# Kernel optimization log

Hardware: AMD Instinct MI355X
Metric: run time of the kernel (lower is better)

## Reference

```python
import jax, jax.numpy as jnp
import numpy as np

N, C, H, W = 8, 256, 128, 128
HW = H * W
NB = 20            # boxes per image
TEMP = 0.5
RATIO = 1.0
IMG_H, IMG_W = 800.0, 800.0  # img_metas[i]['img_shape']


def setup_inputs() -> dict:
    key = jax.random.key(0)
    k1, k2, k3 = jax.random.split(key, 3)
    preds_S = jax.random.normal(k1, (HW, N, C), dtype=jnp.float32)
    preds_T = jax.random.normal(k2, (HW, N, C), dtype=jnp.float32)
    # boxes: random corner pairs in image coords, sorted so x1<=x2, y1<=y2
    u = jax.random.uniform(k3, (N, NB, 4), dtype=jnp.float32)
    x1 = jnp.minimum(u[..., 0], u[..., 2]) * IMG_W
    x2 = jnp.maximum(u[..., 0], u[..., 2]) * IMG_W
    y1 = jnp.minimum(u[..., 1], u[..., 3]) * IMG_H
    y2 = jnp.maximum(u[..., 1], u[..., 3]) * IMG_H
    gt_bboxes = jnp.stack([x1, y1, x2, y2], axis=-1)  # (N, NB, 4)
    return {"preds_S": preds_S, "preds_T": preds_T, "gt_bboxes": gt_bboxes}


def get_attention(preds, temp):
    # preds: (N, C, H, W)
    value = jnp.abs(preds)
    fea_map = value.mean(axis=1)                                   # (N, H, W)
    S_att = (H * W) * jax.nn.softmax((fea_map / temp).reshape(N, -1), axis=1)
    S_att = S_att.reshape(N, H, W)
    channel_map = value.mean(axis=(2, 3))                          # (N, C)
    C_att = C * jax.nn.softmax(channel_map / temp, axis=1)
    return S_att, C_att


def build_masks(gt_bboxes):
    # boxes scaled to feature grid (same math as torch loop, vectorized)
    wmin = jnp.floor(gt_bboxes[..., 0] / IMG_W * W).astype(jnp.int32)  # (N, NB)
    wmax = jnp.ceil(gt_bboxes[..., 2] / IMG_W * W).astype(jnp.int32)
    hmin = jnp.floor(gt_bboxes[..., 1] / IMG_H * H).astype(jnp.int32)
    hmax = jnp.ceil(gt_bboxes[..., 3] / IMG_H * H).astype(jnp.int32)
    area = 1.0 / (hmax + 1 - hmin).astype(jnp.float32) / (wmax + 1 - wmin).astype(jnp.float32)
    hh = jnp.arange(H)[None, None, :, None]
    ww = jnp.arange(W)[None, None, None, :]
    inside = ((hh >= hmin[:, :, None, None]) & (hh <= hmax[:, :, None, None]) &
              (ww >= wmin[:, :, None, None]) & (ww <= wmax[:, :, None, None]))  # (N, NB, H, W)
    # per-box max-scatter == max over boxes of (area where inside else 0)
    Mask_fg = jnp.max(jnp.where(inside, area[:, :, None, None], 0.0), axis=1)  # (N, H, W)
    Mask_bg = (Mask_fg <= 0).astype(jnp.float32)
    s = Mask_bg.sum(axis=(1, 2), keepdims=True)
    Mask_bg = jnp.where(s > 0, Mask_bg / s, Mask_bg)
    return Mask_fg, Mask_bg


def reference(preds_S, preds_T, gt_bboxes):
    # attention from DETACHED teacher features (preds_T.detach() in torch)
    pT_det = jax.lax.stop_gradient(preds_T)
    pT_new = pT_det.reshape(H, W, N, C).transpose(2, 3, 0, 1)  # (N, C, H, W)
    S_t, C_t = get_attention(pT_new, TEMP)

    Mask_fg, Mask_bg = build_masks(gt_bboxes)

    # flatten to the (HW, bs, .) layout of get_fea_loss
    flat = lambda m: m.transpose(1, 2, 0).reshape(HW, N, 1)
    S_t_f = flat(S_t)
    Mfg_f = flat(Mask_fg)
    Mbg_f = flat(Mask_bg)
    C_t_f = C_t[None]  # (1, bs, c) broadcast

    w = jnp.sqrt(S_t_f) * jnp.sqrt(C_t_f)
    fea_t = preds_T * w
    fea_s = preds_S * w
    diff = jnp.abs(fea_s - fea_t)
    fg_loss = jnp.sum(diff * jnp.sqrt(Mfg_f)) / HW
    bg_loss = jnp.sum(diff * jnp.sqrt(Mbg_f)) / HW
    return (fg_loss + bg_loss) * RATIO
```

## Files before the change

### kernel.cpp

```cpp
#include <hip/hip_runtime.h>

#define N_   8
#define C_   256
#define H_   128
#define W_   128
#define HW_  16384
#define NB_  20
constexpr float TEMP  = 0.5f;
constexpr float IMG_W = 800.0f;
constexpr float IMG_H = 800.0f;

__device__ __forceinline__ float waveReduceSum(float v) {
    v += __shfl_xor(v, 32, 64);
    v += __shfl_xor(v, 16, 64);
    v += __shfl_xor(v, 8, 64);
    v += __shfl_xor(v, 4, 64);
    v += __shfl_xor(v, 2, 64);
    v += __shfl_xor(v, 1, 64);
    return v;
}

__global__ __launch_bounds__(256) void k_stats(const float* __restrict__ pT,
                                               float* __restrict__ chan_sum,
                                               float* __restrict__ fea_sum) {
    const int n    = blockIdx.x & 7;
    const int p    = blockIdx.x >> 3;
    const int wave = threadIdx.x >> 6;
    const int lane = threadIdx.x & 63;
    float4 cacc = make_float4(0.f, 0.f, 0.f, 0.f);
    const int hw0 = p * 256 + wave * 64;
    for (int i = 0; i < 64; ++i) {
        const int hw = hw0 + i;
        const float4 v = *(const float4*)(pT + ((size_t)(hw * N_ + n)) * C_ + lane * 4);
        const float ax = fabsf(v.x), ay = fabsf(v.y), az = fabsf(v.z), aw = fabsf(v.w);
        cacc.x += ax; cacc.y += ay; cacc.z += az; cacc.w += aw;
        const float s = waveReduceSum(ax + ay + az + aw);
        if (lane == 0) fea_sum[n * HW_ + hw] = s;
    }
    __shared__ float lds[4][C_];
    lds[wave][lane * 4 + 0] = cacc.x;
    lds[wave][lane * 4 + 1] = cacc.y;
    lds[wave][lane * 4 + 2] = cacc.z;
    lds[wave][lane * 4 + 3] = cacc.w;
    __syncthreads();
    const int c = threadIdx.x;
    const float v = lds[0][c] + lds[1][c] + lds[2][c] + lds[3][c];
    atomicAdd(&chan_sum[n * C_ + c], v);
}

__global__ __launch_bounds__(256) void k_soft(const float* __restrict__ fea_sum,
                                              const float* __restrict__ chan_sum,
                                              float* __restrict__ stats,
                                              float* __restrict__ B) {
    const int n = blockIdx.x;
    const int tid = threadIdx.x;
    __shared__ float red[256];
    float m = -1e30f;
    for (int i = tid; i < HW_; i += 256) m = fmaxf(m, fea_sum[n * HW_ + i]);
    red[tid] = m; __syncthreads();
    for (int s = 128; s > 0; s >>= 1) { if (tid < s) red[tid] = fmaxf(red[tid], red[tid + s]); __syncthreads(); }
    const float smax = red[0] * (1.0f / (C_ * TEMP));
    __syncthreads();
    float acc = 0.f;
    for (int i = tid; i < HW_; i += 256)
        acc += expf(fea_sum[n * HW_ + i] * (1.0f / (C_ * TEMP)) - smax);
    red[tid] = acc; __syncthreads();
    for (int s = 128; s > 0; s >>= 1) { if (tid < s) red[tid] += red[tid + s]; __syncthreads(); }
    const float sden = red[0];
    __syncthreads();
    const float lc = chan_sum[n * C_ + tid] * (1.0f / (HW_ * TEMP));
    red[tid] = lc; __syncthreads();
    for (int s = 128; s > 0; s >>= 1) { if (tid < s) red[tid] = fmaxf(red[tid], red[tid + s]); __syncthreads(); }
    const float cmax = red[0]; __syncthreads();
    const float e = expf(lc - cmax);
    red[tid] = e; __syncthreads();
    for (int s = 128; s > 0; s >>= 1) { if (tid < s) red[tid] += red[tid + s]; __syncthreads(); }
    const float cden = red[0];
    B[n * C_ + tid] = sqrtf((float)C_ * e / cden);
    if (tid == 0) { stats[n] = smax; stats[N_ + n] = sden; }
}

__global__ __launch_bounds__(256) void k_mask(const float* __restrict__ gt,
                                              float* __restrict__ Mfg,
                                              float* __restrict__ bgcnt) {
    const int n = blockIdx.y;
    const int hw = blockIdx.x * 256 + threadIdx.x;
    const int h = hw >> 7, w = hw & 127;
    float fg = 0.f;
    for (int b = 0; b < NB_; ++b) {
        const float* bx = gt + ((size_t)n * NB_ + b) * 4;
        const float x1 = bx[0], y1 = bx[1], x2 = bx[2], y2 = bx[3];
        const int wmin = (int)floorf(x1 / IMG_W * (float)W_);
        const int wmax = (int)ceilf (x2 / IMG_W * (float)W_);
        const int hmin = (int)floorf(y1 / IMG_H * (float)H_);
        const int hmax = (int)ceilf (y2 / IMG_H * (float)H_);
        if (h >= hmin && h <= hmax && w >= wmin && w <= wmax) {
            const float area = 1.0f / (float)(hmax + 1 - hmin) / (float)(wmax + 1 - wmin);
            fg = fmaxf(fg, area);
        }
    }
    Mfg[n * HW_ + hw] = fg;
    __shared__ float red[256];
    red[threadIdx.x] = (fg <= 0.f) ? 1.f : 0.f;
    __syncthreads();
    for (int s = 128; s > 0; s >>= 1) { if (threadIdx.x < s) red[threadIdx.x] += red[threadIdx.x + s]; __syncthreads(); }
    if (threadIdx.x == 0) atomicAdd(&bgcnt[n], red[0]);
}

__global__ __launch_bounds__(256) void k_A(const float* __restrict__ fea_sum,
                                           const float* __restrict__ Mfg,
                                           const float* __restrict__ bgcnt,
                                           const float* __restrict__ stats,
                                           float* __restrict__ A) {
    const int n = blockIdx.y;
    const int hw = blockIdx.x * 256 + threadIdx.x;
    const float smax = stats[n], sden = stats[N_ + n];
    const float logit = fea_sum[n * HW_ + hw] * (1.0f / (C_ * TEMP));
    const float S_att = (float)HW_ * expf(logit - smax) / sden;
    const float fg = Mfg[n * HW_ + hw];
    const float s = bgcnt[n];
    const float bg = (fg <= 0.f) ? ((s > 0.f) ? 1.0f / s : 1.0f) : 0.f;
    A[n * HW_ + hw] = sqrtf(S_att) * (sqrtf(fg) + sqrtf(bg)) * (1.0f / (float)HW_);
}

__global__ __launch_bounds__(256) void k_main(const float* __restrict__ pS,
                                              const float* __restrict__ pT,
                                              const float* __restrict__ A,
                                              const float* __restrict__ B,
                                              float* __restrict__ partials) {
    const int wave = threadIdx.x >> 6, lane = threadIdx.x & 63;
    const int wg = blockIdx.x * 4 + wave;
    const int n = wg & 7;
    const int widx = wg >> 3;
    const float4 B4 = *(const float4*)(B + n * C_ + lane * 4);
    float acc = 0.f;
    const int hw0 = widx * 32;
    for (int i = 0; i < 32; ++i) {
        const int hw = hw0 + i;
        const size_t off = ((size_t)(hw * N_ + n)) * C_ + lane * 4;
        const float4 sv = *(const float4*)(pS + off);
        const float4 tv = *(const float4*)(pT + off);
        const float part = fabsf(sv.x - tv.x) * B4.x + fabsf(sv.y - tv.y) * B4.y +
                           fabsf(sv.z - tv.z) * B4.z + fabsf(sv.w - tv.w) * B4.w;
        acc += A[n * HW_ + hw] * part;
    }
    acc = waveReduceSum(acc);
    __shared__ float red[4];
    if (lane == 0) red[wave] = acc;
    __syncthreads();
    if (threadIdx.x == 0) partials[blockIdx.x] = red[0] + red[1] + red[2] + red[3];
}

__global__ __launch_bounds__(256) void k_final(const float* __restrict__ partials,
                                               float* __restrict__ out) {
    float a = 0.f;
    for (int i = threadIdx.x; i < 1024; i += 256) a += partials[i];
    __shared__ float red[256];
    red[threadIdx.x] = a; __syncthreads();
    for (int s = 128; s > 0; s >>= 1) { if (threadIdx.x < s) red[threadIdx.x] += red[threadIdx.x + s]; __syncthreads(); }
    if (threadIdx.x == 0) out[0] = red[0];
}

extern "C" void kernel_launch(void* const* d_in, const int* in_sizes, int n_in,
                              void* d_out, int out_size, void* d_ws, size_t ws_size,
                              hipStream_t stream) {
    const float* pS = (const float*)d_in[0];
    const float* pT = (const float*)d_in[1];
    const float* gt = (const float*)d_in[2];
    float* ws = (float*)d_ws;

    float* chan_sum = ws;
    float* bgcnt    = ws + 2048;
    float* stats    = ws + 2056;
    float* fea_sum  = ws + 4096;
    float* Mfg      = fea_sum + N_ * HW_;
    float* A        = Mfg + N_ * HW_;
    float* B        = A + N_ * HW_;
    float* partials = B + N_ * C_;

    hipMemsetAsync(ws, 0, 2056 * sizeof(float), stream);

    k_stats<<<512, 256, 0, stream>>>(pT, chan_sum, fea_sum);
    k_soft<<<N_, 256, 0, stream>>>(fea_sum, chan_sum, stats, B);
    k_mask<<<dim3(HW_ / 256, N_), 256, 0, stream>>>(gt, Mfg, bgcnt);
    k_A<<<dim3(HW_ / 256, N_), 256, 0, stream>>>(fea_sum, Mfg, bgcnt, stats, A);
    k_main<<<1024, 256, 0, stream>>>(pS, pT, A, B, partials);
    k_final<<<1, 256, 0, stream>>>(partials, (float*)d_out);
}
```

Before: 338.9 us.

## Fuse mask and attention prep into stats/main kernels, parallelize softmax reductions

Mask construction moves into the stats kernel, and the per-row attention weight is now computed inline in the main kernel, so two separate kernels and the A buffer are gone. The spatial max is tracked with an atomicMax on the float bit pattern, which is valid because the sums are non-negative, and the softmax denominator is split across 64 blocks instead of 8. The stats kernel replaces the per-row full wave reduction with a transposed shuffle that reduces four rows together. Grids grow to 2048 blocks with smaller per-wave work to improve latency hiding, at the cost of more atomics and redundant exp/sqrt per lane in the main kernel.

Measured after the change: 390.3 us. 15.2% more time.

```diff
diff --git a/kernel.cpp b/kernel.cpp
--- a/kernel.cpp
+++ b/kernel.cpp
@@ -20,129 +20,154 @@
     return v;
 }
 
-__global__ __launch_bounds__(256) void k_stats(const float* __restrict__ pT,
-                                               float* __restrict__ chan_sum,
-                                               float* __restrict__ fea_sum) {
-    const int n    = blockIdx.x & 7;
-    const int p    = blockIdx.x >> 3;
-    const int wave = threadIdx.x >> 6;
-    const int lane = threadIdx.x & 63;
+__global__ __launch_bounds__(256, 4) void k_stats(const float* __restrict__ pT,
+                                                  const float* __restrict__ gt,
+                                                  float* __restrict__ chan_sum,
+                                                  float* __restrict__ fea_sum,
+                                                  unsigned int* __restrict__ smax_bits,
+                                                  float* __restrict__ Mfg,
+                                                  float* __restrict__ bgcnt) {
+    const int n     = blockIdx.x & 7;
+    const int chunk = blockIdx.x >> 3;
+    const int wave  = threadIdx.x >> 6;
+    const int lane  = threadIdx.x & 63;
+    const int hwb   = chunk * 64;
+    const int hw0   = hwb + wave * 16;
+
     float4 cacc = make_float4(0.f, 0.f, 0.f, 0.f);
-    const int hw0 = p * 256 + wave * 64;
-    for (int i = 0; i < 64; ++i) {
-        const int hw = hw0 + i;
-        const float4 v = *(const float4*)(pT + ((size_t)(hw * N_ + n)) * C_ + lane * 4);
-        const float ax = fabsf(v.x), ay = fabsf(v.y), az = fabsf(v.z), aw = fabsf(v.w);
-        cacc.x += ax; cacc.y += ay; cacc.z += az; cacc.w += aw;
-        const float s = waveReduceSum(ax + ay + az + aw);
-        if (lane == 0) fea_sum[n * HW_ + hw] = s;
+    float vmax = 0.f;
+    #pragma unroll
+    for (int g = 0; g < 4; ++g) {
+        const int r = hw0 + g * 4;
+        float p[4];
+        #pragma unroll
+        for (int j = 0; j < 4; ++j) {
+            const float4 v = *(const float4*)(pT + ((size_t)((r + j) * N_ + n)) * C_ + lane * 4);
+            const float ax = fabsf(v.x), ay = fabsf(v.y), az = fabsf(v.z), aw = fabsf(v.w);
+            cacc.x += ax; cacc.y += ay; cacc.z += az; cacc.w += aw;
+            p[j] = ax + ay + az + aw;
+        }
+        float a01 = (lane & 32) ? p[1] : p[0];
+        float b01 = (lane & 32) ? p[0] : p[1];
+        const float u01 = a01 + __shfl_xor(b01, 32, 64);
+        float a23 = (lane & 32) ? p[3] : p[2];
+        float b23 = (lane & 32) ? p[2] : p[3];
+        const float u23 = a23 + __shfl_xor(b23, 32, 64);
+        float aq = (lane & 16) ? u23 : u01;
+        float bq = (lane & 16) ? u01 : u23;
+        float u = aq + __shfl_xor(bq, 16, 64);
+        u += __shfl_xor(u, 8, 64);
+        u += __shfl_xor(u, 4, 64);
+        u += __shfl_xor(u, 2, 64);
+        u += __shfl_xor(u, 1, 64);
+        vmax = fmaxf(vmax, u);
+        if ((lane & 15) == 0) {
+            const int q = lane >> 4;
+            const int row = ((q & 1) << 1) | (q >> 1);
+            fea_sum[n * HW_ + r + row] = u;
+        }
     }
+    vmax = fmaxf(vmax, __shfl_xor(vmax, 16, 64));
+    vmax = fmaxf(vmax, __shfl_xor(vmax, 32, 64));
+    if (lane == 0) atomicMax(&smax_bits[n], __float_as_uint(vmax));
+
     __shared__ float lds[4][C_];
-    lds[wave][lane * 4 + 0] = cacc.x;
-    lds[wave][lane * 4 + 1] = cacc.y;
-    lds[wave][lane * 4 + 2] = cacc.z;
-    lds[wave][lane * 4 + 3] = cacc.w;
+    ((float4*)lds[wave])[lane] = cacc;
     __syncthreads();
     const int c = threadIdx.x;
-    const float v = lds[0][c] + lds[1][c] + lds[2][c] + lds[3][c];
-    atomicAdd(&chan_sum[n * C_ + c], v);
+    const float cs = lds[0][c] + lds[1][c] + lds[2][c] + lds[3][c];
+    atomicAdd(&chan_sum[n * C_ + c], cs);
+
+    if (threadIdx.x < 64) {
+        const int hw = hwb + threadIdx.x;
+        const int h = hw >> 7, w = hw & 127;
+        float fg = 0.f;
+        for (int b = 0; b < NB_; ++b) {
+            const float* bx = gt + ((size_t)n * NB_ + b) * 4;
+            const float x1 = bx[0], y1 = bx[1], x2 = bx[2], y2 = bx[3];
+            const int wmin = (int)floorf(x1 / IMG_W * (float)W_);
+            const int wmax = (int)ceilf (x2 / IMG_W * (float)W_);
+            const int hmin = (int)floorf(y1 / IMG_H * (float)H_);
+            const int hmax = (int)ceilf (y2 / IMG_H * (float)H_);
+            if (h >= hmin && h <= hmax && w >= wmin && w <= wmax) {
+                const float area = 1.0f / (float)(hmax + 1 - hmin) / (float)(wmax + 1 - wmin);
+                fg = fmaxf(fg, area);
+            }
+        }
+        Mfg[n * HW_ + hw] = fg;
+        const unsigned long long m = __ballot(fg <= 0.f);
+        if (threadIdx.x == 0) atomicAdd(&bgcnt[n], (float)__popcll(m));
+    }
 }
 
 __global__ __launch_bounds__(256) void k_soft(const float* __restrict__ fea_sum,
                                               const float* __restrict__ chan_sum,
-                                              float* __restrict__ stats,
+                                              const unsigned int* __restrict__ smax_bits,
+                                              float* __restrict__ sden_part,
                                               float* __restrict__ B) {
-    const int n = blockIdx.x;
+    const int n   = blockIdx.x >> 3;
+    const int sub = blockIdx.x & 7;
     const int tid = threadIdx.x;
     __shared__ float red[256];
-    float m = -1e30f;
-    for (int i = tid; i < HW_; i += 256) m = fmaxf(m, fea_sum[n * HW_ + i]);
-    red[tid] = m; __syncthreads();
-    for (int s = 128; s > 0; s >>= 1) { if (tid < s) red[tid] = fmaxf(red[tid], red[tid + s]); __syncthreads(); }
-    const float smax = red[0] * (1.0f / (C_ * TEMP));
-    __syncthreads();
+    const float sm = __uint_as_float(smax_bits[n]) * (1.0f / (C_ * TEMP));
     float acc = 0.f;
-    for (int i = tid; i < HW_; i += 256)
-        acc += expf(fea_sum[n * HW_ + i] * (1.0f / (C_ * TEMP)) - smax);
+    const int base = n * HW_ + sub * 2048;
+    #pragma unroll
+    for (int k = 0; k < 8; ++k)
+        acc += expf(fea_sum[base + k * 256 + tid] * (1.0f / (C_ * TEMP)) - sm);
     red[tid] = acc; __syncthreads();
     for (int s = 128; s > 0; s >>= 1) { if (tid < s) red[tid] += red[tid + s]; __syncthreads(); }
-    const float sden = red[0];
+    if (tid == 0) sden_part[blockIdx.x] = red[0];
+
+    if (blockIdx.x >= 8) return;
     __syncthreads();
-    const float lc = chan_sum[n * C_ + tid] * (1.0f / (HW_ * TEMP));
+    const int n2 = blockIdx.x;
+    const float lc = chan_sum[n2 * C_ + tid] * (1.0f / (HW_ * TEMP));
     red[tid] = lc; __syncthreads();
     for (int s = 128; s > 0; s >>= 1) { if (tid < s) red[tid] = fmaxf(red[tid], red[tid + s]); __syncthreads(); }
     const float cmax = red[0]; __syncthreads();
     const float e = expf(lc - cmax);
     red[tid] = e; __syncthreads();
     for (int s = 128; s > 0; s >>= 1) { if (tid < s) red[tid] += red[tid + s]; __syncthreads(); }
-    const float cden = red[0];
-    B[n * C_ + tid] = sqrtf((float)C_ * e / cden);
-    if (tid == 0) { stats[n] = smax; stats[N_ + n] = sden; }
-}
-
-__global__ __launch_bounds__(256) void k_mask(const float* __restrict__ gt,
-                                              float* __restrict__ Mfg,
-                                              float* __restrict__ bgcnt) {
-    const int n = blockIdx.y;
-    const int hw = blockIdx.x * 256 + threadIdx.x;
-    const int h = hw >> 7, w = hw & 127;
-    float fg = 0.f;
-    for (int b = 0; b < NB_; ++b) {
-        const float* bx = gt + ((size_t)n * NB_ + b) * 4;
-        const float x1 = bx[0], y1 = bx[1], x2 = bx[2], y2 = bx[3];
-        const int wmin = (int)floorf(x1 / IMG_W * (float)W_);
-        const int wmax = (int)ceilf (x2 / IMG_W * (float)W_);
-        const int hmin = (int)floorf(y1 / IMG_H * (float)H_);
-        const int hmax = (int)ceilf (y2 / IMG_H * (float)H_);
-        if (h >= hmin && h <= hmax && w >= wmin && w <= wmax) {
-            const float area = 1.0f / (float)(hmax + 1 - hmin) / (float)(wmax + 1 - wmin);
-            fg = fmaxf(fg, area);
-        }
-    }
-    Mfg[n * HW_ + hw] = fg;
-    __shared__ float red[256];
-    red[threadIdx.x] = (fg <= 0.f) ? 1.f : 0.f;
-    __syncthreads();
-    for (int s = 128; s > 0; s >>= 1) { if (threadIdx.x < s) red[threadIdx.x] += red[threadIdx.x + s]; __syncthreads(); }
-    if (threadIdx.x == 0) atomicAdd(&bgcnt[n], red[0]);
-}
-
-__global__ __launch_bounds__(256) void k_A(const float* __restrict__ fea_sum,
-                                           const float* __restrict__ Mfg,
-                                           const float* __restrict__ bgcnt,
-                                           const float* __restrict__ stats,
-                                           float* __restrict__ A) {
-    const int n = blockIdx.y;
-    const int hw = blockIdx.x * 256 + threadIdx.x;
-    const float smax = stats[n], sden = stats[N_ + n];
-    const float logit = fea_sum[n * HW_ + hw] * (1.0f / (C_ * TEMP));
-    const float S_att = (float)HW_ * expf(logit - smax) / sden;
-    const float fg = Mfg[n * HW_ + hw];
-    const float s = bgcnt[n];
-    const float bg = (fg <= 0.f) ? ((s > 0.f) ? 1.0f / s : 1.0f) : 0.f;
-    A[n * HW_ + hw] = sqrtf(S_att) * (sqrtf(fg) + sqrtf(bg)) * (1.0f / (float)HW_);
-}
-
-__global__ __launch_bounds__(256) void k_main(const float* __restrict__ pS,
-                                              const float* __restrict__ pT,
-                                              const float* __restrict__ A,
-                                              const float* __restrict__ B,
-                                              float* __restrict__ partials) {
+    B[n2 * C_ + tid] = sqrtf((float)C_ * e / red[0]);
+}
+
+__global__ __launch_bounds__(256, 4) void k_main(const float* __restrict__ pS,
+                                                 const float* __restrict__ pT,
+                                                 const float* __restrict__ fea_sum,
+                                                 const float* __restrict__ Mfg,
+                                                 const float* __restrict__ bgcnt,
+                                                 const unsigned int* __restrict__ smax_bits,
+                                                 const float* __restrict__ sden_part,
+                                                 const float* __restrict__ B,
+                                                 float* __restrict__ partials) {
     const int wave = threadIdx.x >> 6, lane = threadIdx.x & 63;
-    const int wg = blockIdx.x * 4 + wave;
-    const int n = wg & 7;
+    const int wg   = blockIdx.x * 4 + wave;
+    const int n    = wg & 7;
     const int widx = wg >> 3;
+    const int hw0  = widx * 16;
+    const float sm = __uint_as_float(smax_bits[n]) * (1.0f / (C_ * TEMP));
+    float sden = 0.f;
+    #pragma unroll
+    for (int j = 0; j < 8; ++j) sden += sden_part[n * 8 + j];
+    const float bgs   = bgcnt[n];
+    const float bginv = (bgs > 0.f) ? 1.0f / bgs : 1.0f;
     const float4 B4 = *(const float4*)(B + n * C_ + lane * 4);
     float acc = 0.f;
-    const int hw0 = widx * 32;
-    for (int i = 0; i < 32; ++i) {
+    #pragma unroll 4
+    for (int i = 0; i < 16; ++i) {
         const int hw = hw0 + i;
+        const float fs = fea_sum[n * HW_ + hw];
+        const float fg = Mfg[n * HW_ + hw];
+        const float S_att = (float)HW_ * expf(fs * (1.0f / (C_ * TEMP)) - sm) / sden;
+        const float bg = (fg <= 0.f) ? bginv : 0.f;
+        const float a_row = sqrtf(S_att) * (sqrtf(fg) + sqrtf(bg)) * (1.0f / (float)HW_);
         const size_t off = ((size_t)(hw * N_ + n)) * C_ + lane * 4;
         const float4 sv = *(const float4*)(pS + off);
         const float4 tv = *(const float4*)(pT + off);
         const float part = fabsf(sv.x - tv.x) * B4.x + fabsf(sv.y - tv.y) * B4.y +
                            fabsf(sv.z - tv.z) * B4.z + fabsf(sv.w - tv.w) * B4.w;
-        acc += A[n * HW_ + hw] * part;
+        acc += a_row * part;
     }
     acc = waveReduceSum(acc);
     __shared__ float red[4];
@@ -154,7 +179,7 @@
 __global__ __launch_bounds__(256) void k_final(const float* __restrict__ partials,
                                                float* __restrict__ out) {
     float a = 0.f;
-    for (int i = threadIdx.x; i < 1024; i += 256) a += partials[i];
+    for (int i = threadIdx.x; i < 2048; i += 256) a += partials[i];
     __shared__ float red[256];
     red[threadIdx.x] = a; __syncthreads();
     for (int s = 128; s > 0; s >>= 1) { if (threadIdx.x < s) red[threadIdx.x] += red[threadIdx.x + s]; __syncthreads(); }
@@ -169,21 +194,19 @@
     const float* gt = (const float*)d_in[2];
     float* ws = (float*)d_ws;
 
-    float* chan_sum = ws;
-    float* bgcnt    = ws + 2048;
-    float* stats    = ws + 2056;
-    float* fea_sum  = ws + 4096;
-    float* Mfg      = fea_sum + N_ * HW_;
-    float* A        = Mfg + N_ * HW_;
-    float* B        = A + N_ * HW_;
-    float* partials = B + N_ * C_;
-
-    hipMemsetAsync(ws, 0, 2056 * sizeof(float), stream);
-
-    k_stats<<<512, 256, 0, stream>>>(pT, chan_sum, fea_sum);
-    k_soft<<<N_, 256, 0, stream>>>(fea_sum, chan_sum, stats, B);
-    k_mask<<<dim3(HW_ / 256, N_), 256, 0, stream>>>(gt, Mfg, bgcnt);
-    k_A<<<dim3(HW_ / 256, N_), 256, 0, stream>>>(fea_sum, Mfg, bgcnt, stats, A);
-    k_main<<<1024, 256, 0, stream>>>(pS, pT, A, B, partials);
-    k_final<<<1, 256, 0, stream>>>(partials, (float*)d_out);
-}
+    float* chan_sum      = ws;
+    float* bgcnt         = ws + 2048;
+    unsigned int* smax   = (unsigned int*)(ws + 2056);
+    float* sden_part     = ws + 2064;
+    float* fea_sum       = ws + 4096;
+    float* Mfg           = fea_sum + N_ * HW_;
+    float* B             = Mfg + N_ * HW_;
+    float* partials      = B + N_ * C_;
+
+    hipMemsetAsync(ws, 0, 2064 * sizeof(float), stream);
+
+    k_stats<<<2048, 256, 0, stream>>>(pT, gt, chan_sum, fea_sum, smax, Mfg, bgcnt);
+    k_soft <<<64,   256, 0, stream>>>(fea_sum, chan_sum, smax, sden_part, B);
+    k_main <<<2048, 256, 0, stream>>>(pS, pT, fea_sum, Mfg, bgcnt, smax, sden_part, B, partials);
+    k_final<<<1,    256, 0, stream>>>(partials, (float*)d_out);
+}
```
